# Kernel optimization log

Measured on AMD Instinct MI355X. Metric: run time of the kernel, lower is better.

The kernel has to match this reference:

```python
import jax, jax.numpy as jnp
import numpy as np

N_NODES = 50000
N_EDGES = 800000
NODE_IN = 128
EDGE_IN = 16
HIDDEN = 128
OUT = 128


def setup_inputs() -> dict:
    key = jax.random.key(0)
    ks = jax.random.split(key, 8)
    x = jax.random.normal(ks[0], (N_NODES, NODE_IN), dtype=jnp.float32)
    edge_index = jax.random.randint(ks[1], (2, N_EDGES), 0, N_NODES, dtype=jnp.int64)
    edge_attr = jax.random.normal(ks[2], (N_EDGES, EDGE_IN), dtype=jnp.float32)
    # Linear weights stored as [in, out] (torch Linear weight is [out, in]); kaiming-ish scale
    s1 = 1.0 / np.sqrt(NODE_IN + EDGE_IN)
    s2 = 1.0 / np.sqrt(HIDDEN + EDGE_IN)
    W1 = jax.random.uniform(ks[3], (NODE_IN + EDGE_IN, HIDDEN), jnp.float32, -s1, s1)
    b1 = jnp.zeros((HIDDEN,), jnp.float32)
    W2 = jax.random.uniform(ks[4], (HIDDEN + EDGE_IN, OUT), jnp.float32, -s2, s2)
    b2 = jnp.zeros((OUT,), jnp.float32)
    return {"x": x, "edge_index": edge_index, "edge_attr": edge_attr,
            "W1": W1, "b1": b1, "W2": W2, "b2": b2}


def _edge_conv(x, src, dst, edge_attr, W, b, num_nodes):
    # message: lin(cat([x_j, edge_attr])) == x_j @ W_x + edge_attr @ W_e
    d = x.shape[1]
    Wx, We = W[:d], W[d:]
    msg = x[src] @ Wx + edge_attr @ We           # [E, out]
    aggr = jax.ops.segment_sum(msg, dst, num_segments=num_nodes)  # scatter-add
    return aggr + b


def reference(x, edge_index, edge_attr, W1, b1, W2, b2):
    src, dst = edge_index[0], edge_index[1]
    h = jax.nn.relu(_edge_conv(x, src, dst, edge_attr, W1, b1, N_NODES))
    return _edge_conv(h, src, dst, edge_attr, W2, b2, N_NODES)
```

## Files before the change

### kernel.cpp

```cpp
#include <hip/hip_runtime.h>

#define N_NODES 50000
#define N_EDGES 800000
#define F_NODE 128
#define F_EDGE 16

#define BUCK_SH 6
#define NBUCK ((N_NODES + 63) >> BUCK_SH)
#define NPART 8
#define CAP_PART 304
#define BCUR_STRIDE 16
#define CAP_BUCKET 1216

#define CONV_BLOCKS ((N_NODES * 32 + 255) / 256)
#define SCAT_BLOCKS ((N_EDGES + 255) / 256)
#define NB128 ((N_NODES + 3) / 4)
#define NB16  ((N_NODES + 3) / 4)

#define PERM_T 512

__device__ __forceinline__ unsigned int bf16_rn(float f) {
    unsigned int u = __float_as_uint(f);
    unsigned int r = ((u >> 16) & 1u) + 0x7fffu;
    return (u + r) >> 16;
}
__device__ __forceinline__ unsigned int pack_bf16(float a, float b) {
    return bf16_rn(a) | (bf16_rn(b) << 16);
}
__device__ __forceinline__ float bf_lo(unsigned int u) { return __uint_as_float(u << 16); }
__device__ __forceinline__ float bf_hi(unsigned int u) { return __uint_as_float(u & 0xffff0000u); }

__global__ __launch_bounds__(256) void convert_and_scatter(
    const float4* __restrict__ x4, uint2* __restrict__ xb2,
    const int* __restrict__ src, const int* __restrict__ dst,
    int* __restrict__ bcur, unsigned long long* __restrict__ temp)
{
    if (blockIdx.x < CONV_BLOCKS) {
        int i = blockIdx.x * 256 + threadIdx.x;
        float4 v = x4[i];
        uint2 o;
        o.x = pack_bf16(v.x, v.y);
        o.y = pack_bf16(v.z, v.w);
        xb2[i] = o;
    } else {
        int e = (int)(blockIdx.x - CONV_BLOCKS) * 256 + threadIdx.x;
        if (e >= N_EDGES) return;
        int d = dst[e];
        int b = d >> BUCK_SH;
        int dl = d & 63;
        int cell = b * NPART + (blockIdx.x & (NPART - 1));
        int pos = atomicAdd(&bcur[cell * BCUR_STRIDE], 1);
        if (pos < CAP_PART)
            temp[(size_t)cell * CAP_PART + pos] =
                (unsigned long long)src[e] |
                ((unsigned long long)e  << 17) |
                ((unsigned long long)dl << 37);
    }
}

__global__ __launch_bounds__(PERM_T) void bucket_permute(
    const unsigned long long* __restrict__ temp,
    const int* __restrict__ bcur,
    int2* __restrict__ rs2,
    int* __restrict__ csr_src, int* __restrict__ csr_eid)
{
    __shared__ int cnt[64];
    __shared__ int scn[64];
    __shared__ int cnt2[64];
    __shared__ int mm[NPART];
    int b = blockIdx.x;
    int tid = threadIdx.x;
    int node0 = b << BUCK_SH;
    int nn = min(64, N_NODES - node0);
    if (tid < 64) { cnt[tid] = 0; cnt2[tid] = 0; }
    if (tid >= 64 && tid < 64 + NPART) {
        int part = tid - 64;
        int m = bcur[(b * NPART + part) * BCUR_STRIDE];
        mm[part] = m > CAP_PART ? CAP_PART : m;
    }
    __syncthreads();
    const int base = b * CAP_BUCKET;
    const size_t tb0 = (size_t)(b * NPART) * CAP_PART;

    for (int idx = tid; idx < NPART * CAP_PART; idx += PERM_T) {
        int part = idx / CAP_PART;
        int i = idx - part * CAP_PART;
        if (i < mm[part]) {
            int dl = (int)(temp[tb0 + idx] >> 37);
            atomicAdd(&cnt[dl], 1);
        }
    }
    __syncthreads();

    if (tid < 64) scn[tid] = cnt[tid];
    __syncthreads();
    for (int o = 1; o < 64; o <<= 1) {
        int v = 0;
        if (tid < 64 && tid >= o) v = scn[tid - o];
        __syncthreads();
        if (tid < 64) scn[tid] += v;
        __syncthreads();
    }
    if (tid < nn)
        rs2[node0 + tid] = make_int2(base + scn[tid] - cnt[tid], base + scn[tid]);

    for (int idx = tid; idx < NPART * CAP_PART; idx += PERM_T) {
        int part = idx / CAP_PART;
        int i = idx - part * CAP_PART;
        if (i < mm[part]) {
            unsigned long long v = temp[tb0 + idx];
            int s  = (int)(v & 0x1FFFF);
            int ei = (int)((v >> 17) & 0xFFFFF);
            int dl = (int)(v >> 37);
            int pos = base + (scn[dl] - cnt[dl]) + atomicAdd(&cnt2[dl], 1);
            csr_src[pos] = s;
            csr_eid[pos] = ei;
        }
    }
}

__device__ __forceinline__ void agg128_body(const unsigned int* __restrict__ xb,
                                            const int2* __restrict__ rs2,
                                            const int* __restrict__ csr_src,
                                            float* __restrict__ xa,
                                            int bid) {
    int gid = bid * 256 + (int)threadIdx.x;
    int n = gid >> 6;
    int lane = threadIdx.x & 63;
    if (n >= N_NODES) return;
    int2 be = rs2[n];
    int beg = be.x, end = be.y;
    float a0 = 0.f, a1 = 0.f;
    int i = beg;
    for (; i + 8 <= end; i += 8) {
        int s[8];
        #pragma unroll
        for (int t = 0; t < 8; ++t) s[t] = csr_src[i + t];
        unsigned int u[8];
        #pragma unroll
        for (int t = 0; t < 8; ++t) u[t] = xb[(size_t)s[t] * 64 + lane];
        #pragma unroll
        for (int t = 0; t < 8; ++t) { a0 += bf_lo(u[t]); a1 += bf_hi(u[t]); }
    }
    for (; i + 4 <= end; i += 4) {
        int s[4];
        #pragma unroll
        for (int t = 0; t < 4; ++t) s[t] = csr_src[i + t];
        unsigned int u[4];
        #pragma unroll
        for (int t = 0; t < 4; ++t) u[t] = xb[(size_t)s[t] * 64 + lane];
        #pragma unroll
        for (int t = 0; t < 4; ++t) { a0 += bf_lo(u[t]); a1 += bf_hi(u[t]); }
    }
    for (; i < end; ++i) {
        unsigned int u = xb[(size_t)csr_src[i] * 64 + lane];
        a0 += bf_lo(u);
        a1 += bf_hi(u);
    }
    *(float2*)(xa + (size_t)n * F_NODE + lane * 2) = make_float2(a0, a1);
}

__device__ __forceinline__ void agg16_body(const float4* __restrict__ eattr4,
                                           const int2* __restrict__ rs2,
                                           const int* __restrict__ csr_eid,
                                           float* __restrict__ eagg,
                                           int bid) {
    int gid = bid * 256 + (int)threadIdx.x;
    int n = gid >> 6;
    int lane = threadIdx.x & 63;
    int sub = lane >> 2;
    int j4  = lane & 3;
    if (n >= N_NODES) return;
    int2 be = rs2[n];
    int beg = be.x, end = be.y;
    float4 acc = make_float4(0.f, 0.f, 0.f, 0.f);
    for (int i = beg + sub; i < end; i += 16) {
        int eid = csr_eid[i];
        float4 v = eattr4[(size_t)eid * 4 + j4];
        acc.x += v.x; acc.y += v.y; acc.z += v.z; acc.w += v.w;
    }
    #pragma unroll
    for (int m = 4; m <= 32; m <<= 1) {
        acc.x += __shfl_xor(acc.x, m, 64);
        acc.y += __shfl_xor(acc.y, m, 64);
        acc.z += __shfl_xor(acc.z, m, 64);
        acc.w += __shfl_xor(acc.w, m, 64);
    }
    if (sub == 0) *(float4*)(eagg + (size_t)n * F_EDGE + j4 * 4) = acc;
}

__global__ __launch_bounds__(256) void agg_combo(const unsigned int* __restrict__ xb,
                                                 const float4* __restrict__ eattr4,
                                                 const int2* __restrict__ rs2,
                                                 const int* __restrict__ csr_src,
                                                 const int* __restrict__ csr_eid,
                                                 float* __restrict__ xa,
                                                 float* __restrict__ eagg) {
    if (blockIdx.x < NB128)
        agg128_body(xb, rs2, csr_src, xa, blockIdx.x);
    else
        agg16_body(eattr4, rs2, csr_eid, eagg, blockIdx.x - NB128);
}

__global__ __launch_bounds__(256) void agg128_bf16(const unsigned int* __restrict__ xb,
                                                   const int2* __restrict__ rs2,
                                                   const int* __restrict__ csr_src,
                                                   float* __restrict__ xa) {
    agg128_body(xb, rs2, csr_src, xa, blockIdx.x);
}

#define BM 64
#define BK 16
#define LDA (BM + 4)
#define LDB (128 + 4)

__global__ __launch_bounds__(256) void layer_gemm(
    const float* xa,
    const float* __restrict__ eagg,
    const float* __restrict__ W,
    const float* __restrict__ bias,
    float* out_f32,
    unsigned int* __restrict__ out_bf,
    int do_relu, int out_bf16)
{
    __shared__ float As[BK][LDA];
    __shared__ float Bs[BK][LDB];
    const int tid = threadIdx.x;
    const int bm = blockIdx.x * BM;

    const int tcol = (tid & 15) * 8;
    const int trow = (tid >> 4) * 4;

    const int lm = tid >> 2;
    const int lk = (tid & 3) * 4;
    const int bk = tid >> 4;
    const int bj = (tid & 15) * 8;

    const int row = bm + lm;
    const bool rowok = row < N_NODES;

    float acc[4][8];
    #pragma unroll
    for (int i = 0; i < 4; ++i)
        #pragma unroll
        for (int j = 0; j < 8; ++j) acc[i][j] = 0.f;

    for (int k0 = 0; k0 < 144; k0 += BK) {
        float4 av = make_float4(0.f, 0.f, 0.f, 0.f);
        if (rowok) {
            if (k0 < F_NODE)
                av = *(const float4*)(xa + (size_t)row * F_NODE + k0 + lk);
            else
                av = *(const float4*)(eagg + (size_t)row * F_EDGE + lk);
        }
        As[lk + 0][lm] = av.x;
        As[lk + 1][lm] = av.y;
        As[lk + 2][lm] = av.z;
        As[lk + 3][lm] = av.w;

        const float4 b0 = *(const float4*)(W + (size_t)(k0 + bk) * 128 + bj);
        const float4 b1 = *(const float4*)(W + (size_t)(k0 + bk) * 128 + bj + 4);
        *(float4*)(&Bs[bk][bj])     = b0;
        *(float4*)(&Bs[bk][bj + 4]) = b1;
        __syncthreads();

        #pragma unroll
        for (int k = 0; k < BK; ++k) {
            float a0 = As[k][trow + 0];
            float a1 = As[k][trow + 1];
            float a2 = As[k][trow + 2];
            float a3 = As[k][trow + 3];
            float bv[8];
            #pragma unroll
            for (int j = 0; j < 8; ++j) bv[j] = Bs[k][tcol + j];
            #pragma unroll
            for (int j = 0; j < 8; ++j) {
                acc[0][j] = fmaf(a0, bv[j], acc[0][j]);
                acc[1][j] = fmaf(a1, bv[j], acc[1][j]);
                acc[2][j] = fmaf(a2, bv[j], acc[2][j]);
                acc[3][j] = fmaf(a3, bv[j], acc[3][j]);
            }
        }
        __syncthreads();
    }

    float4 bb0 = *(const float4*)(bias + tcol);
    float4 bb1 = *(const float4*)(bias + tcol + 4);
    #pragma unroll
    for (int i = 0; i < 4; ++i) {
        int r = bm + trow + i;
        if (r >= N_NODES) break;
        float v[8];
        v[0] = acc[i][0] + bb0.x; v[1] = acc[i][1] + bb0.y;
        v[2] = acc[i][2] + bb0.z; v[3] = acc[i][3] + bb0.w;
        v[4] = acc[i][4] + bb1.x; v[5] = acc[i][5] + bb1.y;
        v[6] = acc[i][6] + bb1.z; v[7] = acc[i][7] + bb1.w;
        if (do_relu) {
            #pragma unroll
            for (int j = 0; j < 8; ++j) v[j] = fmaxf(v[j], 0.f);
        }
        if (out_bf16) {
            uint4 s;
            s.x = pack_bf16(v[0], v[1]);
            s.y = pack_bf16(v[2], v[3]);
            s.z = pack_bf16(v[4], v[5]);
            s.w = pack_bf16(v[6], v[7]);
            *(uint4*)(out_bf + (size_t)r * 64 + tcol / 2) = s;
        } else {
            *(float4*)(out_f32 + (size_t)r * 128 + tcol)     = make_float4(v[0], v[1], v[2], v[3]);
            *(float4*)(out_f32 + (size_t)r * 128 + tcol + 4) = make_float4(v[4], v[5], v[6], v[7]);
        }
    }
}

static inline char* align16(char* p) {
    return (char*)(((uintptr_t)p + 15) & ~(uintptr_t)15);
}

extern "C" void kernel_launch(void* const* d_in, const int* in_sizes, int n_in,
                              void* d_out, int out_size, void* d_ws, size_t ws_size,
                              hipStream_t stream) {
    const float* x     = (const float*)d_in[0];
    const int*   eidx  = (const int*)  d_in[1];
    const float* eattr = (const float*)d_in[2];
    const float* W1    = (const float*)d_in[3];
    const float* b1    = (const float*)d_in[4];
    const float* W2    = (const float*)d_in[5];
    const float* b2    = (const float*)d_in[6];
    float* out = (float*)d_out;

    const int* srcv = eidx;
    const int* dstv = eidx + N_EDGES;

    unsigned long long* temp = (unsigned long long*)d_out;

    char* p = (char*)d_ws;
    unsigned int* xbhb = (unsigned int*)p;  p += (size_t)N_NODES * 64 * 4;
    float* eagg        = (float*)p;         p += (size_t)N_NODES * F_EDGE * 4;
    int* csr_src = (int*)p;                 p += (size_t)NBUCK * CAP_BUCKET * 4;
    int* csr_eid = (int*)p;                 p += (size_t)NBUCK * CAP_BUCKET * 4;
    int2* rs2    = (int2*)p;                p += (size_t)N_NODES * 8;
    p = align16(p);
    int* bcur    = (int*)p;                 p += (size_t)NBUCK * NPART * BCUR_STRIDE * 4;

    float* xa = out;

    hipMemsetAsync(bcur, 0, (size_t)NBUCK * NPART * BCUR_STRIDE * 4, stream);

    convert_and_scatter<<<CONV_BLOCKS + SCAT_BLOCKS, 256, 0, stream>>>(
        (const float4*)x, (uint2*)xbhb, srcv, dstv, bcur, temp);

    bucket_permute<<<NBUCK, PERM_T, 0, stream>>>(temp, bcur, rs2, csr_src, csr_eid);

    agg_combo<<<NB128 + NB16, 256, 0, stream>>>(
        xbhb, (const float4*)eattr, rs2, csr_src, csr_eid, xa, eagg);

    layer_gemm<<<(N_NODES + BM - 1) / BM, 256, 0, stream>>>(
        xa, eagg, W1, b1, (float*)nullptr, xbhb, 1, 1);

    agg128_bf16<<<NB128, 256, 0, stream>>>(xbhb, rs2, csr_src, xa);

    layer_gemm<<<(N_NODES + BM - 1) / BM, 256, 0, stream>>>(
        xa, eagg, W2, b2, out, (unsigned int*)nullptr, 0, 0);
}
```

Before: 309.4 us.

## Replace FP32 SIMT GEMM with bf16 MFMA GEMM over packed bf16 activations

After: 363.0 us. +17.4%, slower.

```diff
diff --git a/kernel.cpp b/kernel.cpp
--- a/kernel.cpp
+++ b/kernel.cpp
@@ -19,6 +19,9 @@
 
 #define PERM_T 512
 
+#define KA 160
+#define WT_PAD 168
+
 __device__ __forceinline__ unsigned int bf16_rn(float f) {
     unsigned int u = __float_as_uint(f);
     unsigned int r = ((u >> 16) & 1u) + 0x7fffu;
@@ -29,6 +32,9 @@
 }
 __device__ __forceinline__ float bf_lo(unsigned int u) { return __uint_as_float(u << 16); }
 __device__ __forceinline__ float bf_hi(unsigned int u) { return __uint_as_float(u & 0xffff0000u); }
+
+typedef __attribute__((ext_vector_type(8))) short bf16x8;
+typedef __attribute__((ext_vector_type(4))) float f32x4;
 
 __global__ __launch_bounds__(256) void convert_and_scatter(
     const float4* __restrict__ x4, uint2* __restrict__ xb2,
@@ -122,7 +128,7 @@
 __device__ __forceinline__ void agg128_body(const unsigned int* __restrict__ xb,
                                             const int2* __restrict__ rs2,
                                             const int* __restrict__ csr_src,
-                                            float* __restrict__ xa,
+                                            unsigned short* __restrict__ A16,
                                             int bid) {
     int gid = bid * 256 + (int)threadIdx.x;
     int n = gid >> 6;
@@ -157,13 +163,13 @@
         a0 += bf_lo(u);
         a1 += bf_hi(u);
     }
-    *(float2*)(xa + (size_t)n * F_NODE + lane * 2) = make_float2(a0, a1);
+    *(unsigned int*)(A16 + (size_t)n * KA + lane * 2) = pack_bf16(a0, a1);
 }
 
 __device__ __forceinline__ void agg16_body(const float4* __restrict__ eattr4,
                                            const int2* __restrict__ rs2,
                                            const int* __restrict__ csr_eid,
-                                           float* __restrict__ eagg,
+                                           unsigned short* __restrict__ A16,
                                            int bid) {
     int gid = bid * 256 + (int)threadIdx.x;
     int n = gid >> 6;
@@ -186,7 +192,12 @@
         acc.z += __shfl_xor(acc.z, m, 64);
         acc.w += __shfl_xor(acc.w, m, 64);
     }
-    if (sub == 0) *(float4*)(eagg + (size_t)n * F_EDGE + j4 * 4) = acc;
+    if (sub == 0) {
+        *(uint2*)(A16 + (size_t)n * KA + 128 + j4 * 4) =
+            make_uint2(pack_bf16(acc.x, acc.y), pack_bf16(acc.z, acc.w));
+    } else if (sub == 2) {
+        *(uint2*)(A16 + (size_t)n * KA + 144 + j4 * 4) = make_uint2(0u, 0u);
+    }
 }
 
 __global__ __launch_bounds__(256) void agg_combo(const unsigned int* __restrict__ xb,
@@ -194,121 +205,79 @@
                                                  const int2* __restrict__ rs2,
                                                  const int* __restrict__ csr_src,
                                                  const int* __restrict__ csr_eid,
-                                                 float* __restrict__ xa,
-                                                 float* __restrict__ eagg) {
+                                                 unsigned short* __restrict__ A16) {
     if (blockIdx.x < NB128)
-        agg128_body(xb, rs2, csr_src, xa, blockIdx.x);
+        agg128_body(xb, rs2, csr_src, A16, blockIdx.x);
     else
-        agg16_body(eattr4, rs2, csr_eid, eagg, blockIdx.x - NB128);
+        agg16_body(eattr4, rs2, csr_eid, A16, blockIdx.x - NB128);
 }
 
 __global__ __launch_bounds__(256) void agg128_bf16(const unsigned int* __restrict__ xb,
                                                    const int2* __restrict__ rs2,
                                                    const int* __restrict__ csr_src,
-                                                   float* __restrict__ xa) {
-    agg128_body(xb, rs2, csr_src, xa, blockIdx.x);
-}
-
-#define BM 64
-#define BK 16
-#define LDA (BM + 4)
-#define LDB (128 + 4)
-
-__global__ __launch_bounds__(256) void layer_gemm(
-    const float* xa,
-    const float* __restrict__ eagg,
+                                                   unsigned short* __restrict__ A16) {
+    agg128_body(xb, rs2, csr_src, A16, blockIdx.x);
+}
+
+__global__ __launch_bounds__(256) void layer_gemm_mfma(
+    const unsigned short* __restrict__ A,
     const float* __restrict__ W,
     const float* __restrict__ bias,
-    float* out_f32,
-    unsigned int* __restrict__ out_bf,
+    float* __restrict__ out_f32,
+    unsigned short* __restrict__ out_bf,
     int do_relu, int out_bf16)
 {
-    __shared__ float As[BK][LDA];
-    __shared__ float Bs[BK][LDB];
+    __shared__ unsigned short Wt[128][WT_PAD];
     const int tid = threadIdx.x;
-    const int bm = blockIdx.x * BM;
-
-    const int tcol = (tid & 15) * 8;
-    const int trow = (tid >> 4) * 4;
-
-    const int lm = tid >> 2;
-    const int lk = (tid & 3) * 4;
-    const int bk = tid >> 4;
-    const int bj = (tid & 15) * 8;
-
-    const int row = bm + lm;
-    const bool rowok = row < N_NODES;
-
-    float acc[4][8];
-    #pragma unroll
-    for (int i = 0; i < 4; ++i)
-        #pragma unroll
-        for (int j = 0; j < 8; ++j) acc[i][j] = 0.f;
-
-    for (int k0 = 0; k0 < 144; k0 += BK) {
-        float4 av = make_float4(0.f, 0.f, 0.f, 0.f);
-        if (rowok) {
-            if (k0 < F_NODE)
-                av = *(const float4*)(xa + (size_t)row * F_NODE + k0 + lk);
+
+    for (int i = tid; i < 128 * KA; i += 256) {
+        int k = i >> 7, col = i & 127;
+        float v = (k < 144) ? W[k * 128 + col] : 0.f;
+        Wt[col][k] = (unsigned short)bf16_rn(v);
+    }
+    __syncthreads();
+
+    const int w    = tid >> 6;
+    const int lane = tid & 63;
+    const int l15  = lane & 15;
+    const int kg   = lane >> 4;
+    const int row0 = blockIdx.x * 64 + w * 16;
+    const int arow = row0 + l15;
+    const int rcl  = arow < N_NODES ? arow : N_NODES - 1;
+
+    bf16x8 af[5];
+    #pragma unroll
+    for (int kk = 0; kk < 5; ++kk)
+        af[kk] = *(const bf16x8*)(A + (size_t)rcl * KA + kk * 32 + kg * 8);
+
+    f32x4 acc[8];
+    #pragma unroll
+    for (int nt = 0; nt < 8; ++nt)
+        acc[nt] = (f32x4){0.f, 0.f, 0.f, 0.f};
+
+    #pragma unroll
+    for (int kk = 0; kk < 5; ++kk) {
+        #pragma unroll
+        for (int nt = 0; nt < 8; ++nt) {
+            bf16x8 bf = *(const bf16x8*)(&Wt[nt * 16 + l15][kk * 32 + kg * 8]);
+            acc[nt] = __builtin_amdgcn_mfma_f32_16x16x32_bf16(af[kk], bf, acc[nt], 0, 0, 0);
+        }
+    }
+
+    #pragma unroll
+    for (int nt = 0; nt < 8; ++nt) {
+        int col = nt * 16 + l15;
+        float bv = bias[col];
+        #pragma unroll
+        for (int r = 0; r < 4; ++r) {
+            int orow = row0 + kg * 4 + r;
+            if (orow >= N_NODES) continue;
+            float v = acc[nt][r] + bv;
+            if (do_relu) v = fmaxf(v, 0.f);
+            if (out_bf16)
+                out_bf[(size_t)orow * 128 + col] = (unsigned short)bf16_rn(v);
             else
-                av = *(const float4*)(eagg + (size_t)row * F_EDGE + lk);
-        }
-        As[lk + 0][lm] = av.x;
-        As[lk + 1][lm] = av.y;
-        As[lk + 2][lm] = av.z;
-        As[lk + 3][lm] = av.w;
-
-        const float4 b0 = *(const float4*)(W + (size_t)(k0 + bk) * 128 + bj);
-        const float4 b1 = *(const float4*)(W + (size_t)(k0 + bk) * 128 + bj + 4);
-        *(float4*)(&Bs[bk][bj])     = b0;
-        *(float4*)(&Bs[bk][bj + 4]) = b1;
-        __syncthreads();
-
-        #pragma unroll
-        for (int k = 0; k < BK; ++k) {
-            float a0 = As[k][trow + 0];
-            float a1 = As[k][trow + 1];
-            float a2 = As[k][trow + 2];
-            float a3 = As[k][trow + 3];
-            float bv[8];
-            #pragma unroll
-            for (int j = 0; j < 8; ++j) bv[j] = Bs[k][tcol + j];
-            #pragma unroll
-            for (int j = 0; j < 8; ++j) {
-                acc[0][j] = fmaf(a0, bv[j], acc[0][j]);
-                acc[1][j] = fmaf(a1, bv[j], acc[1][j]);
-                acc[2][j] = fmaf(a2, bv[j], acc[2][j]);
-                acc[3][j] = fmaf(a3, bv[j], acc[3][j]);
-            }
-        }
-        __syncthreads();
-    }
-
-    float4 bb0 = *(const float4*)(bias + tcol);
-    float4 bb1 = *(const float4*)(bias + tcol + 4);
-    #pragma unroll
-    for (int i = 0; i < 4; ++i) {
-        int r = bm + trow + i;
-        if (r >= N_NODES) break;
-        float v[8];
-        v[0] = acc[i][0] + bb0.x; v[1] = acc[i][1] + bb0.y;
-        v[2] = acc[i][2] + bb0.z; v[3] = acc[i][3] + bb0.w;
-        v[4] = acc[i][4] + bb1.x; v[5] = acc[i][5] + bb1.y;
-        v[6] = acc[i][6] + bb1.z; v[7] = acc[i][7] + bb1.w;
-        if (do_relu) {
-            #pragma unroll
-            for (int j = 0; j < 8; ++j) v[j] = fmaxf(v[j], 0.f);
-        }
-        if (out_bf16) {
-            uint4 s;
-            s.x = pack_bf16(v[0], v[1]);
-            s.y = pack_bf16(v[2], v[3]);
-            s.z = pack_bf16(v[4], v[5]);
-            s.w = pack_bf16(v[6], v[7]);
-            *(uint4*)(out_bf + (size_t)r * 64 + tcol / 2) = s;
-        } else {
-            *(float4*)(out_f32 + (size_t)r * 128 + tcol)     = make_float4(v[0], v[1], v[2], v[3]);
-            *(float4*)(out_f32 + (size_t)r * 128 + tcol + 4) = make_float4(v[4], v[5], v[6], v[7]);
+                out_f32[(size_t)orow * 128 + col] = v;
         }
     }
 }
@@ -335,16 +304,14 @@
     unsigned long long* temp = (unsigned long long*)d_out;
 
     char* p = (char*)d_ws;
-    unsigned int* xbhb = (unsigned int*)p;  p += (size_t)N_NODES * 64 * 4;
-    float* eagg        = (float*)p;         p += (size_t)N_NODES * F_EDGE * 4;
+    unsigned int* xbhb   = (unsigned int*)p;   p += (size_t)N_NODES * 64 * 4;
+    unsigned short* A16  = (unsigned short*)p; p += (size_t)N_NODES * KA * 2;
     int* csr_src = (int*)p;                 p += (size_t)NBUCK * CAP_BUCKET * 4;
     int* csr_eid = (int*)p;                 p += (size_t)NBUCK * CAP_BUCKET * 4;
     int2* rs2    = (int2*)p;                p += (size_t)N_NODES * 8;
     p = align16(p);
     int* bcur    = (int*)p;                 p += (size_t)NBUCK * NPART * BCUR_STRIDE * 4;
 
-    float* xa = out;
-
     hipMemsetAsync(bcur, 0, (size_t)NBUCK * NPART * BCUR_STRIDE * 4, stream);
 
     convert_and_scatter<<<CONV_BLOCKS + SCAT_BLOCKS, 256, 0, stream>>>(
@@ -353,13 +320,13 @@
     bucket_permute<<<NBUCK, PERM_T, 0, stream>>>(temp, bcur, rs2, csr_src, csr_eid);
 
     agg_combo<<<NB128 + NB16, 256, 0, stream>>>(
-        xbhb, (const float4*)eattr, rs2, csr_src, csr_eid, xa, eagg);
-
-    layer_gemm<<<(N_NODES + BM - 1) / BM, 256, 0, stream>>>(
-        xa, eagg, W1, b1, (float*)nullptr, xbhb, 1, 1);
-
-    agg128_bf16<<<NB128, 256, 0, stream>>>(xbhb, rs2, csr_src, xa);
-
-    layer_gemm<<<(N_NODES + BM - 1) / BM, 256, 0, stream>>>(
-        xa, eagg, W2, b2, out, (unsigned int*)nullptr, 0, 0);
-}
+        xbhb, (const float4*)eattr, rs2, csr_src, csr_eid, A16);
+
+    layer_gemm_mfma<<<(N_NODES + 63) / 64, 256, 0, stream>>>(
+        A16, W1, b1, (float*)nullptr, (unsigned short*)xbhb, 1, 1);
+
+    agg128_bf16<<<NB128, 256, 0, stream>>>(xbhb, rs2, csr_src, A16);
+
+    layer_gemm_mfma<<<(N_NODES + 63) / 64, 256, 0, stream>>>(
+        A16, W2, b2, out, (unsigned short*)nullptr, 0, 0);
+}
```
